# Performance work log

Measured on AMD Instinct MI355X. Metric: run time of the kernel, lower is better.

## Reference

```python
import jax, jax.numpy as jnp
import numpy as np

B, N = 8, 512
EMBED, EDGE_D, FLAG_D = 256, 32, 32
NODE_NUM, EDGE_NUM, FLAG_NUM = 20000, 16, 4
IN_DIM = 2 * EMBED + 2 * FLAG_D + EDGE_D  # concat order: [head_emb, tail_emb, head_flag, tail_flag, edge]
NEG = -1e12


def setup_inputs() -> dict:
    key = jax.random.key(0)
    ks = jax.random.split(key, 16)
    s = 0.05
    return {
        "adjacent_matrix": jax.random.randint(ks[0], (B, N, N), 0, 2, dtype=jnp.int32),
        "head_nodes": jax.random.randint(ks[1], (B, N), 0, NODE_NUM, dtype=jnp.int32),
        "head_flag_bit_matrix": jax.random.randint(ks[2], (B, N), 0, FLAG_NUM, dtype=jnp.int32),
        "edge_type_matrix": jax.random.randint(ks[3], (B, N, N), 0, EDGE_NUM, dtype=jnp.int32),
        "node_emb": jax.random.normal(ks[4], (NODE_NUM, EMBED)) * s,
        "edge_emb": jax.random.normal(ks[5], (EDGE_NUM, EDGE_D)) * s,
        "flag_emb": jax.random.normal(ks[6], (FLAG_NUM, FLAG_D)) * s,
        "t1_w": jax.random.normal(ks[7], (EMBED, EMBED)) * s,
        "t1_b": jax.random.normal(ks[8], (EMBED,)) * s,
        "w1": jax.random.normal(ks[9], (IN_DIM,)) * s,
        "b1": jax.random.normal(ks[10], ()) * s,
        "t2_w": jax.random.normal(ks[11], (EMBED, EMBED)) * s,
        "t2_b": jax.random.normal(ks[12], (EMBED,)) * s,
        "w2": jax.random.normal(ks[13], (IN_DIM,)) * s,
        "b2": jax.random.normal(ks[14], ()) * s,
    }


def _leaky_relu(x):
    return jnp.where(x > 0, x, 0.1 * x)


def _gat_layer(h, f, e, adj, w, b):
    # Decompose Linear(concat([h_i, h_j, f_i, f_j, e_ij])) into per-part dot
    # products summed by broadcasting -> avoids the [B,N,N,IN_DIM] concat.
    D, F = h.shape[-1], f.shape[-1]
    wh, wt = w[:D], w[D:2 * D]
    wfh, wft = w[2 * D:2 * D + F], w[2 * D + F:2 * D + 2 * F]
    we = w[2 * D + 2 * F:]
    logit = ((h @ wh)[:, :, None] + (h @ wt)[:, None, :]
             + (f @ wfh)[:, :, None] + (f @ wft)[:, None, :]
             + jnp.einsum('bije,e->bij', e, we) + b)  # [B,N,N]
    logit = _leaky_relu(logit)
    logit = jnp.where(adj == 0, NEG, logit)
    att = jax.nn.softmax(logit, axis=1)  # softmax over head axis i
    # out[b,j] = sum_i att[b,i,j] * h[b,i]   (== bmm(att^T, h))
    return jnp.einsum('bij,bid->bjd', att, h)


def reference(adjacent_matrix, head_nodes, head_flag_bit_matrix, edge_type_matrix,
              node_emb, edge_emb, flag_emb,
              t1_w, t1_b, w1, b1, t2_w, t2_b, w2, b2):
    h = node_emb[head_nodes] @ t1_w.T + t1_b          # [B,N,D] (t1 projection)
    f = flag_emb[head_flag_bit_matrix]                # [B,N,F]
    e = edge_emb[edge_type_matrix]                    # [B,N,N,E]
    t = _gat_layer(h, f, e, adjacent_matrix, w1, b1)  # layer 1 aggregate
    t = jax.nn.sigmoid(t)
    h2 = t @ t2_w.T + t2_b                            # t2 projection
    return _gat_layer(h2, f, e, adjacent_matrix, w2, b2)
```

## Files before the change

kernel.cpp:

```cpp
#include <hip/hip_runtime.h>
#include <hip/hip_bf16.h>

#define BB 8
#define NN 512
#define DD 256
#define NROWS (BB*NN)
#define JT 16

using bf16x8 = __attribute__((ext_vector_type(8))) short;
using f32x4  = __attribute__((ext_vector_type(4))) float;
typedef unsigned short us_t;

__device__ __forceinline__ us_t f2bf(float x) {
    union { float f; unsigned int u; } v; v.f = x;
    unsigned int r = (v.u + 0x7fffu + ((v.u >> 16) & 1u)) >> 16;
    return (us_t)r;
}

__global__ __launch_bounds__(256) void prep_w(
    const float* __restrict__ w1f, const float* __restrict__ w2f,
    us_t* __restrict__ o1, us_t* __restrict__ o2)
{
    int i = blockIdx.x*1024 + threadIdx.x*4;
    float4 a = *(const float4*)(w1f + i);
    float4 b = *(const float4*)(w2f + i);
    ushort4 u;
    u.x = f2bf(a.x); u.y = f2bf(a.y); u.z = f2bf(a.z); u.w = f2bf(a.w);
    *(ushort4*)&o1[i] = u;
    u.x = f2bf(b.x); u.y = f2bf(b.y); u.z = f2bf(b.z); u.w = f2bf(b.w);
    *(ushort4*)&o2[i] = u;
}

__device__ __forceinline__ void lin_body(
    int bid, int t,
    const us_t* __restrict__ Wbf, const float* __restrict__ bias,
    const float* __restrict__ Xf, const int* __restrict__ idx,
    const float* __restrict__ wvec, const int* __restrict__ flagidx,
    const float* __restrict__ flag_emb,
    us_t* __restrict__ hT, float* __restrict__ aout, float* __restrict__ cout,
    float* redA, float* redC)
{
    const int wave = t >> 6, lane = t & 63;
    const int lrow = lane & 15, kg = lane >> 4;
    const int r0 = bid * 16;
    const int dw = wave * 64;

    const int arow = r0 + lrow;
    const int nid = idx ? idx[arow] : arow;

    f32x4 acc[4];
    #pragma unroll
    for (int n = 0; n < 4; ++n) acc[n] = (f32x4){0.f, 0.f, 0.f, 0.f};

    const float4* xr = (const float4*)(Xf + (size_t)nid * DD);
    #pragma unroll
    for (int ks = 0; ks < DD/32; ++ks) {
        float4 xa = xr[ks*8 + kg*2];
        float4 xb = xr[ks*8 + kg*2 + 1];
        bf16x8 af;
        af[0] = (short)f2bf(xa.x); af[1] = (short)f2bf(xa.y);
        af[2] = (short)f2bf(xa.z); af[3] = (short)f2bf(xa.w);
        af[4] = (short)f2bf(xb.x); af[5] = (short)f2bf(xb.y);
        af[6] = (short)f2bf(xb.z); af[7] = (short)f2bf(xb.w);
        #pragma unroll
        for (int n = 0; n < 4; ++n) {
            bf16x8 bfr = *(const bf16x8*)(Wbf + (size_t)(dw + n*16 + lrow)*DD
                                           + ks*32 + kg*8);
            acc[n] = __builtin_amdgcn_mfma_f32_16x16x32_bf16(af, bfr, acc[n], 0, 0, 0);
        }
    }

    const int b  = r0 >> 9;
    const int i0 = (r0 & 511) + kg*4;
    float pa[4] = {0.f,0.f,0.f,0.f}, pc[4] = {0.f,0.f,0.f,0.f};
    #pragma unroll
    for (int n = 0; n < 4; ++n) {
        int d = dw + n*16 + lrow;
        float bv = bias[d];
        float whd = wvec[d], wtd = wvec[256+d];
        ushort4 u;
        #pragma unroll
        for (int r = 0; r < 4; ++r) {
            float v = acc[n][r] + bv;
            ((us_t*)&u)[r] = f2bf(v);
            pa[r] += v * whd;
            pc[r] += v * wtd;
        }
        *(ushort4*)&hT[(size_t)b*DD*NN + (size_t)d*NN + i0] = u;
    }
    #pragma unroll
    for (int r = 0; r < 4; ++r) {
        #pragma unroll
        for (int m = 1; m < 16; m <<= 1) {
            pa[r] += __shfl_xor(pa[r], m);
            pc[r] += __shfl_xor(pc[r], m);
        }
    }
    if (lrow == 0) {
        #pragma unroll
        for (int r = 0; r < 4; ++r) {
            redA[wave*16 + kg*4 + r] = pa[r];
            redC[wave*16 + kg*4 + r] = pc[r];
        }
    }
    __syncthreads();
    if (t < 128) {
        const int m = t >> 3, sub = t & 7;
        const int fi = flagidx[r0 + m];
        float fa = 0.f, fc = 0.f;
        #pragma unroll
        for (int q = 0; q < 4; ++q) {
            int e = sub*4 + q;
            float fe = flag_emb[fi*32 + e];
            fa += fe * wvec[512 + e];
            fc += fe * wvec[544 + e];
        }
        #pragma unroll
        for (int mm = 1; mm < 8; mm <<= 1) {
            fa += __shfl_xor(fa, mm);
            fc += __shfl_xor(fc, mm);
        }
        if (sub == 0) {
            float sa = fa, sc = fc;
            #pragma unroll
            for (int wv = 0; wv < 4; ++wv) { sa += redA[wv*16 + m]; sc += redC[wv*16 + m]; }
            aout[r0 + m] = sa;
            cout[r0 + m] = sc;
        }
    }
}

__global__ __launch_bounds__(256) void k1(
    const us_t* __restrict__ Wb1, const float* __restrict__ bias1,
    const float* __restrict__ node_emb, const int* __restrict__ head_nodes,
    const float* __restrict__ wvec1, const int* __restrict__ flagidx,
    const float* __restrict__ flag_emb,
    us_t* __restrict__ hT, float* __restrict__ a1, float* __restrict__ c1,
    const int* __restrict__ adj, const int* __restrict__ et,
    unsigned char* __restrict__ pk)
{
    __shared__ float redA[64], redC[64];
    const int blk = blockIdx.x, t = threadIdx.x;
    if (blk < 256) {
        int bid = ((blk & 7) << 5) | (blk >> 3);
        lin_body(bid, t, Wb1, bias1, node_emb, head_nodes,
                 wvec1, flagidx, flag_emb, hT, a1, c1, redA, redC);
    } else {
        int pb = blk - 256;
        int pbid = ((pb & 7) << 8) | (pb >> 3);
        int g = (pbid*256 + t)*4;
        int4 av = *(const int4*)(adj + g);
        int4 ev = *(const int4*)(et + g);
        uchar4 u;
        u.x = (unsigned char)((ev.x&15)|(av.x<<4));
        u.y = (unsigned char)((ev.y&15)|(av.y<<4));
        u.z = (unsigned char)((ev.z&15)|(av.z<<4));
        u.w = (unsigned char)((ev.w&15)|(av.w<<4));
        *(uchar4*)(pk + g) = u;
    }
}

__global__ __launch_bounds__(512) void attn1_lin2(
    const unsigned char* __restrict__ pk,
    const float* __restrict__ edge_emb, const float* __restrict__ w,
    const float* __restrict__ bptr,
    const float* __restrict__ a, const float* __restrict__ c,
    const us_t* __restrict__ hT,
    const us_t* __restrict__ Wb2, const float* __restrict__ bias2,
    const float* __restrict__ wvec2, const int* __restrict__ flagidx,
    const float* __restrict__ flag_emb,
    us_t* __restrict__ hT2, float* __restrict__ a2, float* __restrict__ c2)
{
    __shared__ __align__(16) float p[NN][JT+1];
    __shared__ __align__(16) us_t Pb[JT][NN+8];
    __shared__ __align__(16) us_t Sg[16][DD+8];
    __shared__ float as[NN];
    __shared__ float edot[16];
    __shared__ float cjs[JT];
    __shared__ float redw[8][16];
    __shared__ float mj[JT];
    __shared__ float invden[JT];
    __shared__ float redA[128], redC[128];

    const int t = threadIdx.x;
    const int b  = blockIdx.x & 7;
    const int j0 = (blockIdx.x >> 3) * JT;
    const int wave = t >> 6, lane = t & 63;

    as[t] = a[b*NN + t & 511 ? b*NN + t : b*NN + t];
    as[t] = a[b*NN + t];
    if (t < 16) {
        float s = 0.f;
        for (int e2 = 0; e2 < 32; ++e2)
            s += edge_emb[t*32 + e2] * w[576 + e2];
        edot[t] = s;
    } else if (t < 32) {
        cjs[t-16] = c[b*NN + j0 + (t-16)];
    }
    const float bias = bptr[0];
    __syncthreads();

    const unsigned char* pkb = pk + (size_t)b*NN*NN + j0;
    #pragma unroll
    for (int it = 0; it < 4; ++it) {
        int lid4 = (it*512 + t) * 4;
        int i = lid4 >> 4, jj = lid4 & 15;
        uchar4 u = *(const uchar4*)(pkb + (size_t)i*NN + jj);
        float base = as[i] + bias;
        unsigned char uv[4] = {u.x, u.y, u.z, u.w};
        #pragma unroll
        for (int q = 0; q < 4; ++q) {
            float l = base + cjs[jj+q] + edot[uv[q] & 15];
            l = (l > 0.f) ? l : 0.1f*l;
            p[i][jj+q] = (uv[q] >> 4) ? l : -1.0e30f;
        }
    }
    __syncthreads();

    const int j = t & 15, grp = t >> 4;
    float m = -3.0e38f;
    #pragma unroll
    for (int s = 0; s < 16; ++s) m = fmaxf(m, p[grp + s*32][j]);
    m = fmaxf(m, __shfl_xor(m, 16));
    m = fmaxf(m, __shfl_xor(m, 32));
    if (lane < 16) redw[wave][lane] = m;
    __syncthreads();
    if (t < 16) {
        float mm = redw[0][t];
        #pragma unroll
        for (int wv = 1; wv < 8; ++wv) mm = fmaxf(mm, redw[wv][t]);
        mj[t] = mm;
    }
    __syncthreads();
    const float mmax = mj[j];
    float ssum = 0.f;
    #pragma unroll
    for (int s = 0; s < 16; ++s) {
        float v = __expf(p[grp + s*32][j] - mmax);
        p[grp + s*32][j] = v;
        ssum += v;
    }
    ssum += __shfl_xor(ssum, 16);
    ssum += __shfl_xor(ssum, 32);
    if (lane < 16) redw[wave][lane] = ssum;
    __syncthreads();
    if (t < 16) {
        float sm = redw[0][t];
        #pragma unroll
        for (int wv = 1; wv < 8; ++wv) sm += redw[wv][t];
        invden[t] = 1.f / sm;
    }
    __syncthreads();

    const float inv = invden[j];
    #pragma unroll
    for (int s = 0; s < 8; ++s) {
        int i = grp*2 + s*64;
        ushort2 u;
        u.x = f2bf(p[i  ][j] * inv);
        u.y = f2bf(p[i+1][j] * inv);
        *(ushort2*)&Pb[j][i] = u;
    }
    __syncthreads();

    const int dw = wave * 32;
    const int lrow = lane & 15;
    const int kg   = lane >> 4;
    f32x4 acc[2];
    acc[0] = (f32x4){0.f,0.f,0.f,0.f};
    acc[1] = (f32x4){0.f,0.f,0.f,0.f};

    const us_t* hTb = hT + (size_t)b*DD*NN;
    const us_t* hp[2];
    hp[0] = hTb + (size_t)(dw + lrow)*NN + kg*8;
    hp[1] = hTb + (size_t)(dw + 16 + lrow)*NN + kg*8;

    #pragma unroll 4
    for (int ks = 0; ks < NN/32; ++ks) {
        int k0 = ks*32;
        bf16x8 afr = *(const bf16x8*)&Pb[lrow][kg*8 + k0];
        #pragma unroll
        for (int n = 0; n < 2; ++n) {
            bf16x8 bfr = *(const bf16x8*)(hp[n] + k0);
            acc[n] = __builtin_amdgcn_mfma_f32_16x16x32_bf16(afr, bfr, acc[n], 0, 0, 0);
        }
    }

    #pragma unroll
    for (int n = 0; n < 2; ++n) {
        #pragma unroll
        for (int r = 0; r < 4; ++r) {
            float v = 1.f/(1.f + __expf(-acc[n][r]));
            Sg[kg*4 + r][dw + n*16 + lrow] = f2bf(v);
        }
    }
    __syncthreads();

    f32x4 acc2[2];
    acc2[0] = (f32x4){0.f,0.f,0.f,0.f};
    acc2[1] = (f32x4){0.f,0.f,0.f,0.f};
    #pragma unroll
    for (int ks = 0; ks < DD/32; ++ks) {
        bf16x8 af2 = *(const bf16x8*)&Sg[lrow][ks*32 + kg*8];
        #pragma unroll
        for (int n = 0; n < 2; ++n) {
            bf16x8 bf2 = *(const bf16x8*)(Wb2 + (size_t)(dw + n*16 + lrow)*DD
                                           + ks*32 + kg*8);
            acc2[n] = __builtin_amdgcn_mfma_f32_16x16x32_bf16(af2, bf2, acc2[n], 0, 0, 0);
        }
    }

    const int r0 = b*NN + j0;
    const int i0 = j0 + kg*4;
    float pa[4] = {0.f,0.f,0.f,0.f}, pc[4] = {0.f,0.f,0.f,0.f};
    #pragma unroll
    for (int n = 0; n < 2; ++n) {
        int d = dw + n*16 + lrow;
        float bv = bias2[d];
        float whd = wvec2[d], wtd = wvec2[256+d];
        ushort4 u;
        #pragma unroll
        for (int r = 0; r < 4; ++r) {
            float v = acc2[n][r] + bv;
            ((us_t*)&u)[r] = f2bf(v);
            pa[r] += v * whd;
            pc[r] += v * wtd;
        }
        *(ushort4*)&hT2[(size_t)b*DD*NN + (size_t)d*NN + i0] = u;
    }
    #pragma unroll
    for (int r = 0; r < 4; ++r) {
        #pragma unroll
        for (int mk = 1; mk < 16; mk <<= 1) {
            pa[r] += __shfl_xor(pa[r], mk);
            pc[r] += __shfl_xor(pc[r], mk);
        }
    }
    if (lrow == 0) {
        #pragma unroll
        for (int r = 0; r < 4; ++r) {
            redA[wave*16 + kg*4 + r] = pa[r];
            redC[wave*16 + kg*4 + r] = pc[r];
        }
    }
    __syncthreads();
    if (t < 128) {
        const int mrow = t >> 3, sub = t & 7;
        const int fi = flagidx[r0 + mrow];
        float fa = 0.f, fc = 0.f;
        #pragma unroll
        for (int q = 0; q < 4; ++q) {
            int e = sub*4 + q;
            float fe = flag_emb[fi*32 + e];
            fa += fe * wvec2[512 + e];
            fc += fe * wvec2[544 + e];
        }
        #pragma unroll
        for (int mm = 1; mm < 8; mm <<= 1) {
            fa += __shfl_xor(fa, mm);
            fc += __shfl_xor(fc, mm);
        }
        if (sub == 0) {
            float sa = fa, sc = fc;
            #pragma unroll
            for (int wv = 0; wv < 8; ++wv) { sa += redA[wv*16 + mrow]; sc += redC[wv*16 + mrow]; }
            a2[r0 + mrow] = sa;
            c2[r0 + mrow] = sc;
        }
    }
}

__global__ __launch_bounds__(512) void attn2(
    const unsigned char* __restrict__ pk,
    const float* __restrict__ edge_emb, const float* __restrict__ w,
    const float* __restrict__ bptr,
    const float* __restrict__ a, const float* __restrict__ c,
    const us_t* __restrict__ hT,
    float* __restrict__ outf)
{
    __shared__ __align__(16) float p[NN][JT+1];
    __shared__ __align__(16) us_t Pb[JT][NN+8];
    __shared__ float as[NN];
    __shared__ float edot[16];
    __shared__ float cjs[JT];
    __shared__ float redw[8][16];
    __shared__ float mj[JT];
    __shared__ float invden[JT];

    const int t = threadIdx.x;
    const int b  = blockIdx.x & 7;
    const int j0 = (blockIdx.x >> 3) * JT;
    const int wave = t >> 6, lane = t & 63;

    as[t] = a[b*NN + t];
    if (t < 16) {
        float s = 0.f;
        for (int e2 = 0; e2 < 32; ++e2)
            s += edge_emb[t*32 + e2] * w[576 + e2];
        edot[t] = s;
    } else if (t < 32) {
        cjs[t-16] = c[b*NN + j0 + (t-16)];
    }
    const float bias = bptr[0];
    __syncthreads();

    const unsigned char* pkb = pk + (size_t)b*NN*NN + j0;
    #pragma unroll
    for (int it = 0; it < 4; ++it) {
        int lid4 = (it*512 + t) * 4;
        int i = lid4 >> 4, jj = lid4 & 15;
        uchar4 u = *(const uchar4*)(pkb + (size_t)i*NN + jj);
        float base = as[i] + bias;
        unsigned char uv[4] = {u.x, u.y, u.z, u.w};
        #pragma unroll
        for (int q = 0; q < 4; ++q) {
            float l = base + cjs[jj+q] + edot[uv[q] & 15];
            l = (l > 0.f) ? l : 0.1f*l;
            p[i][jj+q] = (uv[q] >> 4) ? l : -1.0e30f;
        }
    }
    __syncthreads();

    const int j = t & 15, grp = t >> 4;
    float m = -3.0e38f;
    #pragma unroll
    for (int s = 0; s < 16; ++s) m = fmaxf(m, p[grp + s*32][j]);
    m = fmaxf(m, __shfl_xor(m, 16));
    m = fmaxf(m, __shfl_xor(m, 32));
    if (lane < 16) redw[wave][lane] = m;
    __syncthreads();
    if (t < 16) {
        float mm = redw[0][t];
        #pragma unroll
        for (int wv = 1; wv < 8; ++wv) mm = fmaxf(mm, redw[wv][t]);
        mj[t] = mm;
    }
    __syncthreads();
    const float mmax = mj[j];
    float ssum = 0.f;
    #pragma unroll
    for (int s = 0; s < 16; ++s) {
        float v = __expf(p[grp + s*32][j] - mmax);
        p[grp + s*32][j] = v;
        ssum += v;
    }
    ssum += __shfl_xor(ssum, 16);
    ssum += __shfl_xor(ssum, 32);
    if (lane < 16) redw[wave][lane] = ssum;
    __syncthreads();
    if (t < 16) {
        float sm = redw[0][t];
        #pragma unroll
        for (int wv = 1; wv < 8; ++wv) sm += redw[wv][t];
        invden[t] = 1.f / sm;
    }
    __syncthreads();

    const float inv = invden[j];
    #pragma unroll
    for (int s = 0; s < 8; ++s) {
        int i = grp*2 + s*64;
        ushort2 u;
        u.x = f2bf(p[i  ][j] * inv);
        u.y = f2bf(p[i+1][j] * inv);
        *(ushort2*)&Pb[j][i] = u;
    }
    __syncthreads();

    const int dw = wave * 32;
    const int lrow = lane & 15;
    const int kg   = lane >> 4;
    f32x4 acc[2];
    acc[0] = (f32x4){0.f,0.f,0.f,0.f};
    acc[1] = (f32x4){0.f,0.f,0.f,0.f};

    const us_t* hTb = hT + (size_t)b*DD*NN;
    const us_t* hp[2];
    hp[0] = hTb + (size_t)(dw + lrow)*NN + kg*8;
    hp[1] = hTb + (size_t)(dw + 16 + lrow)*NN + kg*8;

    #pragma unroll 4
    for (int ks = 0; ks < NN/32; ++ks) {
        int k0 = ks*32;
        bf16x8 afr = *(const bf16x8*)&Pb[lrow][kg*8 + k0];
        #pragma unroll
        for (int n = 0; n < 2; ++n) {
            bf16x8 bfr = *(const bf16x8*)(hp[n] + k0);
            acc[n] = __builtin_amdgcn_mfma_f32_16x16x32_bf16(afr, bfr, acc[n], 0, 0, 0);
        }
    }

    #pragma unroll
    for (int n = 0; n < 2; ++n) {
        #pragma unroll
        for (int r = 0; r < 4; ++r) {
            int jj = j0 + kg*4 + r;
            int dd = dw + n*16 + lrow;
            outf[(size_t)(b*NN + jj)*DD + dd] = acc[n][r];
        }
    }
}

extern "C" void kernel_launch(void* const* d_in, const int* in_sizes, int n_in,
                              void* d_out, int out_size, void* d_ws, size_t ws_size,
                              hipStream_t stream) {
    (void)in_sizes; (void)n_in; (void)out_size; (void)ws_size;
    const int*   adj       = (const int*)d_in[0];
    const int*   head_nodes= (const int*)d_in[1];
    const int*   head_flag = (const int*)d_in[2];
    const int*   etype     = (const int*)d_in[3];
    const float* node_emb  = (const float*)d_in[4];
    const float* edge_emb  = (const float*)d_in[5];
    const float* flag_emb  = (const float*)d_in[6];
    const float* t1_w      = (const float*)d_in[7];
    const float* t1_b      = (const float*)d_in[8];
    const float* w1        = (const float*)d_in[9];
    const float* b1        = (const float*)d_in[10];
    const float* t2_w      = (const float*)d_in[11];
    const float* t2_b      = (const float*)d_in[12];
    const float* w2        = (const float*)d_in[13];
    const float* b2        = (const float*)d_in[14];

    us_t* hT1 = (us_t*)d_ws;
    us_t* hT2 = hT1 + (size_t)NROWS*DD;
    us_t* Wb1 = hT2 + (size_t)NROWS*DD;
    us_t* Wb2 = Wb1 + (size_t)DD*DD;
    unsigned char* pk = (unsigned char*)(Wb2 + (size_t)DD*DD);
    float* a1 = (float*)(pk + (size_t)BB*NN*NN);
    float* c1 = a1 + NROWS;
    float* a2 = c1 + NROWS;
    float* c2 = a2 + NROWS;

    prep_w<<<DD*DD/1024, 256, 0, stream>>>(t1_w, t2_w, Wb1, Wb2);
    k1<<<256 + BB*NN*NN/1024, 256, 0, stream>>>(
        Wb1, t1_b, node_emb, head_nodes, w1, head_flag, flag_emb,
        hT1, a1, c1, adj, etype, pk);
    attn1_lin2<<<BB*(NN/JT), 512, 0, stream>>>(
        pk, edge_emb, w1, b1, a1, c1, hT1,
        Wb2, t2_b, w2, head_flag, flag_emb, hT2, a2, c2);
    attn2<<<BB*(NN/JT), 512, 0, stream>>>(
        pk, edge_emb, w2, b2, a2, c2, hT2, (float*)d_out);
}
```

Baseline: 48.63 us.

## Fold weight prep into k1 and defer softmax normalization past the matmul

Removes the separate prep_w launch: k1 now converts t1_w from fp32 to bf16 on the fly inside the MFMA loop, and extra blocks convert t2_w. The softmax now keeps logits in registers and writes unnormalized exp values straight to the bf16 P buffer. The 1/denominator is applied after the P·h matmul, which removes one barrier and one LDS pass in both attention kernels. The cost is redundant fp32 weight loads and conversions in every k1 block, plus slightly different rounding because unnormalized values are stored in bf16.

```diff
diff --git a/kernel.cpp b/kernel.cpp
--- a/kernel.cpp
+++ b/kernel.cpp
@@ -17,136 +17,21 @@
     return (us_t)r;
 }
 
-__global__ __launch_bounds__(256) void prep_w(
-    const float* __restrict__ w1f, const float* __restrict__ w2f,
-    us_t* __restrict__ o1, us_t* __restrict__ o2)
-{
-    int i = blockIdx.x*1024 + threadIdx.x*4;
-    float4 a = *(const float4*)(w1f + i);
-    float4 b = *(const float4*)(w2f + i);
-    ushort4 u;
-    u.x = f2bf(a.x); u.y = f2bf(a.y); u.z = f2bf(a.z); u.w = f2bf(a.w);
-    *(ushort4*)&o1[i] = u;
-    u.x = f2bf(b.x); u.y = f2bf(b.y); u.z = f2bf(b.z); u.w = f2bf(b.w);
-    *(ushort4*)&o2[i] = u;
-}
-
-__device__ __forceinline__ void lin_body(
-    int bid, int t,
-    const us_t* __restrict__ Wbf, const float* __restrict__ bias,
-    const float* __restrict__ Xf, const int* __restrict__ idx,
-    const float* __restrict__ wvec, const int* __restrict__ flagidx,
-    const float* __restrict__ flag_emb,
-    us_t* __restrict__ hT, float* __restrict__ aout, float* __restrict__ cout,
-    float* redA, float* redC)
-{
-    const int wave = t >> 6, lane = t & 63;
-    const int lrow = lane & 15, kg = lane >> 4;
-    const int r0 = bid * 16;
-    const int dw = wave * 64;
-
-    const int arow = r0 + lrow;
-    const int nid = idx ? idx[arow] : arow;
-
-    f32x4 acc[4];
-    #pragma unroll
-    for (int n = 0; n < 4; ++n) acc[n] = (f32x4){0.f, 0.f, 0.f, 0.f};
-
-    const float4* xr = (const float4*)(Xf + (size_t)nid * DD);
-    #pragma unroll
-    for (int ks = 0; ks < DD/32; ++ks) {
-        float4 xa = xr[ks*8 + kg*2];
-        float4 xb = xr[ks*8 + kg*2 + 1];
-        bf16x8 af;
-        af[0] = (short)f2bf(xa.x); af[1] = (short)f2bf(xa.y);
-        af[2] = (short)f2bf(xa.z); af[3] = (short)f2bf(xa.w);
-        af[4] = (short)f2bf(xb.x); af[5] = (short)f2bf(xb.y);
-        af[6] = (short)f2bf(xb.z); af[7] = (short)f2bf(xb.w);
-        #pragma unroll
-        for (int n = 0; n < 4; ++n) {
-            bf16x8 bfr = *(const bf16x8*)(Wbf + (size_t)(dw + n*16 + lrow)*DD
-                                           + ks*32 + kg*8);
-            acc[n] = __builtin_amdgcn_mfma_f32_16x16x32_bf16(af, bfr, acc[n], 0, 0, 0);
-        }
-    }
-
-    const int b  = r0 >> 9;
-    const int i0 = (r0 & 511) + kg*4;
-    float pa[4] = {0.f,0.f,0.f,0.f}, pc[4] = {0.f,0.f,0.f,0.f};
-    #pragma unroll
-    for (int n = 0; n < 4; ++n) {
-        int d = dw + n*16 + lrow;
-        float bv = bias[d];
-        float whd = wvec[d], wtd = wvec[256+d];
-        ushort4 u;
-        #pragma unroll
-        for (int r = 0; r < 4; ++r) {
-            float v = acc[n][r] + bv;
-            ((us_t*)&u)[r] = f2bf(v);
-            pa[r] += v * whd;
-            pc[r] += v * wtd;
-        }
-        *(ushort4*)&hT[(size_t)b*DD*NN + (size_t)d*NN + i0] = u;
-    }
-    #pragma unroll
-    for (int r = 0; r < 4; ++r) {
-        #pragma unroll
-        for (int m = 1; m < 16; m <<= 1) {
-            pa[r] += __shfl_xor(pa[r], m);
-            pc[r] += __shfl_xor(pc[r], m);
-        }
-    }
-    if (lrow == 0) {
-        #pragma unroll
-        for (int r = 0; r < 4; ++r) {
-            redA[wave*16 + kg*4 + r] = pa[r];
-            redC[wave*16 + kg*4 + r] = pc[r];
-        }
-    }
-    __syncthreads();
-    if (t < 128) {
-        const int m = t >> 3, sub = t & 7;
-        const int fi = flagidx[r0 + m];
-        float fa = 0.f, fc = 0.f;
-        #pragma unroll
-        for (int q = 0; q < 4; ++q) {
-            int e = sub*4 + q;
-            float fe = flag_emb[fi*32 + e];
-            fa += fe * wvec[512 + e];
-            fc += fe * wvec[544 + e];
-        }
-        #pragma unroll
-        for (int mm = 1; mm < 8; mm <<= 1) {
-            fa += __shfl_xor(fa, mm);
-            fc += __shfl_xor(fc, mm);
-        }
-        if (sub == 0) {
-            float sa = fa, sc = fc;
-            #pragma unroll
-            for (int wv = 0; wv < 4; ++wv) { sa += redA[wv*16 + m]; sc += redC[wv*16 + m]; }
-            aout[r0 + m] = sa;
-            cout[r0 + m] = sc;
-        }
-    }
-}
-
 __global__ __launch_bounds__(256) void k1(
-    const us_t* __restrict__ Wb1, const float* __restrict__ bias1,
+    const float* __restrict__ w1f, const float* __restrict__ bias1,
     const float* __restrict__ node_emb, const int* __restrict__ head_nodes,
     const float* __restrict__ wvec1, const int* __restrict__ flagidx,
     const float* __restrict__ flag_emb,
     us_t* __restrict__ hT, float* __restrict__ a1, float* __restrict__ c1,
+    const float* __restrict__ w2f, us_t* __restrict__ Wb2,
     const int* __restrict__ adj, const int* __restrict__ et,
     unsigned char* __restrict__ pk)
 {
     __shared__ float redA[64], redC[64];
     const int blk = blockIdx.x, t = threadIdx.x;
-    if (blk < 256) {
-        int bid = ((blk & 7) << 5) | (blk >> 3);
-        lin_body(bid, t, Wb1, bias1, node_emb, head_nodes,
-                 wvec1, flagidx, flag_emb, hT, a1, c1, redA, redC);
-    } else {
-        int pb = blk - 256;
+
+    if (blk >= 320) {
+        int pb = blk - 320;
         int pbid = ((pb & 7) << 8) | (pb >> 3);
         int g = (pbid*256 + t)*4;
         int4 av = *(const int4*)(adj + g);
@@ -157,6 +42,111 @@
         u.z = (unsigned char)((ev.z&15)|(av.z<<4));
         u.w = (unsigned char)((ev.w&15)|(av.w<<4));
         *(uchar4*)(pk + g) = u;
+        return;
+    }
+    if (blk >= 256) {
+        int i = (blk - 256)*1024 + t*4;
+        float4 wv = *(const float4*)(w2f + i);
+        ushort4 u;
+        u.x = f2bf(wv.x); u.y = f2bf(wv.y); u.z = f2bf(wv.z); u.w = f2bf(wv.w);
+        *(ushort4*)&Wb2[i] = u;
+        return;
+    }
+
+    const int bid = ((blk & 7) << 5) | (blk >> 3);
+    const int wave = t >> 6, lane = t & 63;
+    const int lrow = lane & 15, kg = lane >> 4;
+    const int r0 = bid * 16;
+    const int dw = wave * 64;
+
+    const int arow = r0 + lrow;
+    const int nid = head_nodes[arow];
+
+    f32x4 acc[4];
+    #pragma unroll
+    for (int n = 0; n < 4; ++n) acc[n] = (f32x4){0.f, 0.f, 0.f, 0.f};
+
+    const float4* xr = (const float4*)(node_emb + (size_t)nid * DD);
+    #pragma unroll
+    for (int ks = 0; ks < DD/32; ++ks) {
+        float4 xa = xr[ks*8 + kg*2];
+        float4 xb = xr[ks*8 + kg*2 + 1];
+        bf16x8 af;
+        af[0] = (short)f2bf(xa.x); af[1] = (short)f2bf(xa.y);
+        af[2] = (short)f2bf(xa.z); af[3] = (short)f2bf(xa.w);
+        af[4] = (short)f2bf(xb.x); af[5] = (short)f2bf(xb.y);
+        af[6] = (short)f2bf(xb.z); af[7] = (short)f2bf(xb.w);
+        #pragma unroll
+        for (int n = 0; n < 4; ++n) {
+            const float4* wr = (const float4*)(w1f + (size_t)(dw + n*16 + lrow)*DD
+                                                + ks*32 + kg*8);
+            float4 wa = wr[0], wb = wr[1];
+            bf16x8 bfr;
+            bfr[0] = (short)f2bf(wa.x); bfr[1] = (short)f2bf(wa.y);
+            bfr[2] = (short)f2bf(wa.z); bfr[3] = (short)f2bf(wa.w);
+            bfr[4] = (short)f2bf(wb.x); bfr[5] = (short)f2bf(wb.y);
+            bfr[6] = (short)f2bf(wb.z); bfr[7] = (short)f2bf(wb.w);
+            acc[n] = __builtin_amdgcn_mfma_f32_16x16x32_bf16(af, bfr, acc[n], 0, 0, 0);
+        }
+    }
+
+    const int b  = r0 >> 9;
+    const int i0 = (r0 & 511) + kg*4;
+    float pa[4] = {0.f,0.f,0.f,0.f}, pc[4] = {0.f,0.f,0.f,0.f};
+    #pragma unroll
+    for (int n = 0; n < 4; ++n) {
+        int d = dw + n*16 + lrow;
+        float bv = bias1[d];
+        float whd = wvec1[d], wtd = wvec1[256+d];
+        ushort4 u;
+        #pragma unroll
+        for (int r = 0; r < 4; ++r) {
+            float v = acc[n][r] + bv;
+            ((us_t*)&u)[r] = f2bf(v);
+            pa[r] += v * whd;
+            pc[r] += v * wtd;
+        }
+        *(ushort4*)&hT[(size_t)b*DD*NN + (size_t)d*NN + i0] = u;
+    }
+    #pragma unroll
+    for (int r = 0; r < 4; ++r) {
+        #pragma unroll
+        for (int m = 1; m < 16; m <<= 1) {
+            pa[r] += __shfl_xor(pa[r], m);
+            pc[r] += __shfl_xor(pc[r], m);
+        }
+    }
+    if (lrow == 0) {
+        #pragma unroll
+        for (int r = 0; r < 4; ++r) {
+            redA[wave*16 + kg*4 + r] = pa[r];
+            redC[wave*16 + kg*4 + r] = pc[r];
+        }
+    }
+    __syncthreads();
+    if (t < 128) {
+        const int m = t >> 3, sub = t & 7;
+        const int fi = flagidx[r0 + m];
+        float fa = 0.f, fc = 0.f;
+        #pragma unroll
+        for (int q = 0; q < 4; ++q) {
+            int e = sub*4 + q;
+            float fe = flag_emb[fi*32 + e];
+            fa += fe * wvec1[512 + e];
+            fc += fe * wvec1[544 + e];
+        }
+        #pragma unroll
+        for (int mm = 1; mm < 8; mm <<= 1) {
+            fa += __shfl_xor(fa, mm);
+            fc += __shfl_xor(fc, mm);
+        }
+        if (sub == 0) {
+            float sa = fa, sc = fc;
+            #pragma unroll
+            for (int wv = 0; wv < 4; ++wv) { sa += redA[wv*16 + m]; sc += redC[wv*16 + m]; }
+            a1[r0 + m] = sa;
+            c1[r0 + m] = sc;
+        }
     }
 }
 
@@ -187,7 +177,6 @@
     const int j0 = (blockIdx.x >> 3) * JT;
     const int wave = t >> 6, lane = t & 63;
 
-    as[t] = a[b*NN + t & 511 ? b*NN + t : b*NN + t];
     as[t] = a[b*NN + t];
     if (t < 16) {
         float s = 0.f;
@@ -218,9 +207,12 @@
     __syncthreads();
 
     const int j = t & 15, grp = t >> 4;
-    float m = -3.0e38f;
-    #pragma unroll
-    for (int s = 0; s < 16; ++s) m = fmaxf(m, p[grp + s*32][j]);
+    float lv[16];
+    #pragma unroll
+    for (int s = 0; s < 16; ++s) lv[s] = p[grp + s*32][j];
+    float m = lv[0];
+    #pragma unroll
+    for (int s = 1; s < 16; ++s) m = fmaxf(m, lv[s]);
     m = fmaxf(m, __shfl_xor(m, 16));
     m = fmaxf(m, __shfl_xor(m, 32));
     if (lane < 16) redw[wave][lane] = m;
@@ -236,8 +228,8 @@
     float ssum = 0.f;
     #pragma unroll
     for (int s = 0; s < 16; ++s) {
-        float v = __expf(p[grp + s*32][j] - mmax);
-        p[grp + s*32][j] = v;
+        float v = __expf(lv[s] - mmax);
+        Pb[j][grp + s*32] = f2bf(v);
         ssum += v;
     }
     ssum += __shfl_xor(ssum, 16);
@@ -249,17 +241,6 @@
         #pragma unroll
         for (int wv = 1; wv < 8; ++wv) sm += redw[wv][t];
         invden[t] = 1.f / sm;
-    }
-    __syncthreads();
-
-    const float inv = invden[j];
-    #pragma unroll
-    for (int s = 0; s < 8; ++s) {
-        int i = grp*2 + s*64;
-        ushort2 u;
-        u.x = f2bf(p[i  ][j] * inv);
-        u.y = f2bf(p[i+1][j] * inv);
-        *(ushort2*)&Pb[j][i] = u;
     }
     __syncthreads();
 
@@ -286,11 +267,14 @@
         }
     }
 
+    float idr[4];
+    #pragma unroll
+    for (int r = 0; r < 4; ++r) idr[r] = invden[kg*4 + r];
     #pragma unroll
     for (int n = 0; n < 2; ++n) {
         #pragma unroll
         for (int r = 0; r < 4; ++r) {
-            float v = 1.f/(1.f + __expf(-acc[n][r]));
+            float v = 1.f/(1.f + __expf(-acc[n][r]*idr[r]));
             Sg[kg*4 + r][dw + n*16 + lrow] = f2bf(v);
         }
     }
@@ -422,9 +406,12 @@
     __syncthreads();
 
     const int j = t & 15, grp = t >> 4;
-    float m = -3.0e38f;
-    #pragma unroll
-    for (int s = 0; s < 16; ++s) m = fmaxf(m, p[grp + s*32][j]);
+    float lv[16];
+    #pragma unroll
+    for (int s = 0; s < 16; ++s) lv[s] = p[grp + s*32][j];
+    float m = lv[0];
+    #pragma unroll
+    for (int s = 1; s < 16; ++s) m = fmaxf(m, lv[s]);
     m = fmaxf(m, __shfl_xor(m, 16));
     m = fmaxf(m, __shfl_xor(m, 32));
     if (lane < 16) redw[wave][lane] = m;
@@ -440,8 +427,8 @@
     float ssum = 0.f;
     #pragma unroll
     for (int s = 0; s < 16; ++s) {
-        float v = __expf(p[grp + s*32][j] - mmax);
-        p[grp + s*32][j] = v;
+        float v = __expf(lv[s] - mmax);
+        Pb[j][grp + s*32] = f2bf(v);
         ssum += v;
     }
     ssum += __shfl_xor(ssum, 16);
@@ -453,17 +440,6 @@
         #pragma unroll
         for (int wv = 1; wv < 8; ++wv) sm += redw[wv][t];
         invden[t] = 1.f / sm;
-    }
-    __syncthreads();
-
-    const float inv = invden[j];
-    #pragma unroll
-    for (int s = 0; s < 8; ++s) {
-        int i = grp*2 + s*64;
-        ushort2 u;
-        u.x = f2bf(p[i  ][j] * inv);
-        u.y = f2bf(p[i+1][j] * inv);
-        *(ushort2*)&Pb[j][i] = u;
     }
     __syncthreads();
 
@@ -490,13 +466,16 @@
         }
     }
 
+    float idr[4];
+    #pragma unroll
+    for (int r = 0; r < 4; ++r) idr[r] = invden[kg*4 + r];
     #pragma unroll
     for (int n = 0; n < 2; ++n) {
         #pragma unroll
         for (int r = 0; r < 4; ++r) {
             int jj = j0 + kg*4 + r;
             int dd = dw + n*16 + lrow;
-            outf[(size_t)(b*NN + jj)*DD + dd] = acc[n][r];
+            outf[(size_t)(b*NN + jj)*DD + dd] = acc[n][r] * idr[r];
         }
     }
 }
@@ -523,18 +502,16 @@
 
     us_t* hT1 = (us_t*)d_ws;
     us_t* hT2 = hT1 + (size_t)NROWS*DD;
-    us_t* Wb1 = hT2 + (size_t)NROWS*DD;
-    us_t* Wb2 = Wb1 + (size_t)DD*DD;
+    us_t* Wb2 = hT2 + (size_t)NROWS*DD;
     unsigned char* pk = (unsigned char*)(Wb2 + (size_t)DD*DD);
     float* a1 = (float*)(pk + (size_t)BB*NN*NN);
     float* c1 = a1 + NROWS;
     float* a2 = c1 + NROWS;
     float* c2 = a2 + NROWS;
 
-    prep_w<<<DD*DD/1024, 256, 0, stream>>>(t1_w, t2_w, Wb1, Wb2);
-    k1<<<256 + BB*NN*NN/1024, 256, 0, stream>>>(
-        Wb1, t1_b, node_emb, head_nodes, w1, head_flag, flag_emb,
-        hT1, a1, c1, adj, etype, pk);
+    k1<<<320 + BB*NN*NN/1024, 256, 0, stream>>>(
+        t1_w, t1_b, node_emb, head_nodes, w1, head_flag, flag_emb,
+        hT1, a1, c1, t2_w, Wb2, adj, etype, pk);
     attn1_lin2<<<BB*(NN/JT), 512, 0, stream>>>(
         pk, edge_emb, w1, b1, a1, c1, hT1,
         Wb2, t2_b, w2, head_flag, flag_emb, hT2, a2, c2);
```

New measurement: 46.35 us. -4.7%, faster.
